# Performance work log

Hardware: AMD Instinct MI355X
Metric: run time of the kernel (lower is better)

Reference implementation:

```python
import jax, jax.numpy as jnp
import numpy as np

J = 8      # number of octaves/scales
Q = 8      # first-order wavelets per octave (Q2 = 1 for second order)
T = 65536  # signal support
EPS = 1e-8
XI_MAX = 0.35  # highest wavelet center frequency (cycles/sample)


def _build_filters(N=T, J_=J, Q_=Q):
    """Morlet-like analytic filterbank defined directly in the Fourier domain."""
    f = np.fft.fftfreq(N)  # normalized freqs in [-0.5, 0.5)
    # first-order: J*Q log-spaced bandpass filters
    xis1 = XI_MAX * 2.0 ** (-np.arange(J_ * Q_) / Q_)
    sig1 = xis1 / Q_
    psi1 = np.exp(-0.5 * ((f[None, :] - xis1[:, None]) / sig1[:, None]) ** 2)
    j1 = np.arange(J_ * Q_) // Q_  # octave index of each first-order filter
    # second-order: one wavelet per octave (Q2=1)
    xis2 = XI_MAX * 2.0 ** (-np.arange(J_).astype(np.float64))
    sig2 = 0.6 * xis2
    psi2 = np.exp(-0.5 * ((f[None, :] - xis2[:, None]) / sig2[:, None]) ** 2)
    # low-pass at scale 2^J
    sig_phi = XI_MAX * 2.0 ** (-J_)
    phi = np.exp(-0.5 * (f / sig_phi) ** 2)
    return (jnp.asarray(psi1, jnp.float32), jnp.asarray(psi2, jnp.float32),
            jnp.asarray(phi, jnp.float32), j1)


def _scatter(x):
    """Order-0/1/2 wavelet scattering: FFT conv -> modulus -> low-pass -> subsample."""
    psi1, psi2, phi, j1 = _build_filters()
    stride = 2 ** J
    xf = jnp.fft.fft(x)  # [B, N] complex64
    lowpass = lambda uf: jnp.real(jnp.fft.ifft(uf * phi))[..., ::stride]
    S0 = lowpass(xf)[:, None, :]                                  # [B, 1, N/2^J]
    U1 = jnp.abs(jnp.fft.ifft(xf[:, None, :] * psi1[None]))      # [B, JQ, N]
    U1f = jnp.fft.fft(U1)
    S1 = lowpass(U1f)                                             # [B, JQ, N/2^J]
    parts = [S0, S1]
    for j2_ in range(J):  # small fixed loop over second-order scales
        sel = j1 < j2_    # static (numpy) frequency-ordering mask
        if not sel.any():
            continue
        U2 = jnp.abs(jnp.fft.ifft(U1f[:, sel] * psi2[j2_]))
        parts.append(lowpass(jnp.fft.fft(U2)))
    return jnp.concatenate(parts, axis=1)  # [B, 289, N/2^J]


def setup_inputs() -> dict:
    key = jax.random.key(0)
    x = jax.random.normal(key, (8, T), dtype=jnp.float32)
    return {"x": x}


def reference(x):
    Sx = _scatter(x)
    # kymatio Scattering1D has no `output_format` attr -> real=Sx, imag=0,
    # then log-magnitude normalization (normalize=True):
    mag = jnp.sqrt(Sx * Sx + EPS)
    real = jnp.log(mag + EPS)
    imag = jnp.zeros_like(real)
    return (real, imag)
```

## Files before the change

kernel.cpp:

```cpp
#include <hip/hip_runtime.h>
#include <hip/hip_fp16.h>
#include <math.h>

#define NN 65536
#define TWO_PI 6.283185307179586f
#define RSTR 264
#define SWZ(m) ((m) ^ (((m) >> 4) & 15))
#define SWZI(m, r) (SWZ(m) ^ ((r) & 12))
#define CTOT 10829824ul

__constant__ int CLO[8]  = {-32768, -15360, -5376, -8192, -8192, -2048, -2048, -2048};
__constant__ int CWW[8]  = {65536, 42240, 16384, 16384, 16384, 4096, 4096, 4096};
__constant__ int CRING[8] = {0, 0, 1, 1, 1, 1, 1, 1};
__constant__ unsigned long COFF[8] = {0ul, 4194304ul, 6897664ul, 7946240ul,
                                      8994816ul, 10043392ul, 10305536ul, 10567680ul};

__device__ __forceinline__ void lds_fence() {
    asm volatile("s_waitcnt lgkmcnt(0)" ::: "memory");
}
__device__ __forceinline__ int rev16(int p) { return ((p & 3) << 2) | (p >> 2); }
__device__ __forceinline__ int rev64(int p) { return ((p & 3) << 4) | (p & 12) | (p >> 4); }

__device__ __forceinline__ int quarter_mask(int klo, int khi)
{
    int qm = 0;
#pragma unroll
    for (int qq = 0; qq < 4; ++qq) {
        int lo_q = 16384 * qq - 255;
        int hi_q = 16384 * qq + 16639;
        bool act;
        if (klo >= 0) act = (hi_q >= klo) && (lo_q <= khi);
        else          act = (lo_q <= khi) || (hi_q >= klo + NN);
        if (act) qm |= (1 << qq);
    }
    return qm;
}

__device__ __forceinline__ void build_tw6(float* twt, int t)
{
    if (t < 16) {
        float s1, c1; __sincosf((TWO_PI / 64.0f) * (float)t, &s1, &c1);
        float c2 = c1 * c1 - s1 * s1, s2 = 2.f * c1 * s1;
        float c3 = c2 * c1 - s2 * s1, s3 = c2 * s1 + s2 * c1;
        float* e = twt + 6 * t;
        e[0] = c1; e[1] = s1; e[2] = c2; e[3] = s2; e[4] = c3; e[5] = s3;
    }
}

template<int SIGN>
__device__ __forceinline__ void fft16(float* xr, float* xi, float* yr, float* yi)
{
    const float S = (SIGN > 0) ? 1.0f : -1.0f;
    const float C8 = 0.92387953251f, S8 = 0.38268343236f, R2 = 0.70710678119f;
#pragma unroll
    for (int n0 = 0; n0 < 4; ++n0) {
        float z0r=xr[n0],    z0i=xi[n0];
        float z1r=xr[n0+4],  z1i=xi[n0+4];
        float z2r=xr[n0+8],  z2i=xi[n0+8];
        float z3r=xr[n0+12], z3i=xi[n0+12];
        float t0r=z0r+z2r, t0i=z0i+z2i;
        float t1r=z0r-z2r, t1i=z0i-z2i;
        float t2r=z1r+z3r, t2i=z1i+z3i;
        float t3r=S*(z1r-z3r), t3i=S*(z1i-z3i);
        xr[n0]=t0r+t2r;      xi[n0]=t0i+t2i;
        xr[n0+4]=t1r-t3i;    xi[n0+4]=t1i+t3r;
        xr[n0+8]=t0r-t2r;    xi[n0+8]=t0i-t2i;
        xr[n0+12]=t1r+t3i;   xi[n0+12]=t1i-t3r;
    }
    {
        const float W1r=C8,  W1i=S*S8;
        const float W2r=R2,  W2i=S*R2;
        const float W3r=S8,  W3i=S*C8;
        const float W6r=-R2, W6i=S*R2;
        const float W9r=-C8, W9i=-S*S8;
#define TWID(idx, wr, wi) { float ar=xr[idx], ai=xi[idx]; xr[idx]=ar*(wr)-ai*(wi); xi[idx]=ar*(wi)+ai*(wr); }
        TWID(5,W1r,W1i)  TWID(9,W2r,W2i)   TWID(13,W3r,W3i)
        TWID(6,W2r,W2i)  { float ar=xr[10], ai=xi[10]; xr[10]=-S*ai; xi[10]=S*ar; } TWID(14,W6r,W6i)
        TWID(7,W3r,W3i)  TWID(11,W6r,W6i)  TWID(15,W9r,W9i)
#undef TWID
    }
#pragma unroll
    for (int p = 0; p < 4; ++p) {
        float z0r=xr[4*p],   z0i=xi[4*p];
        float z1r=xr[4*p+1], z1i=xi[4*p+1];
        float z2r=xr[4*p+2], z2i=xi[4*p+2];
        float z3r=xr[4*p+3], z3i=xi[4*p+3];
        float t0r=z0r+z2r, t0i=z0i+z2i;
        float t1r=z0r-z2r, t1i=z0i-z2i;
        float t2r=z1r+z3r, t2i=z1i+z3i;
        float t3r=S*(z1r-z3r), t3i=S*(z1i-z3i);
        yr[p]=t0r+t2r;     yi[p]=t0i+t2i;
        yr[p+4]=t1r-t3i;   yi[p+4]=t1i+t3r;
        yr[p+8]=t0r-t2r;   yi[p+8]=t0i-t2i;
        yr[p+12]=t1r+t3i;  yi[p+12]=t1i-t3r;
    }
}

template<int SIGN, bool BIGTW, int OUT, bool INREAL, int PADL, int PADR>
__device__ __forceinline__ void fft256_soa(float* rr, float* ri, int u, int n1,
                                           float twrate, float mscale, int cxor, int qmask)
{
    float xr[16], xi[16], yr[16], yi[16];
#pragma unroll
    for (int qq = 0; qq < 4; ++qq) {
        if (qmask & (1 << qq)) {
#pragma unroll
            for (int j = 0; j < 4; ++j) {
                int b = qq * 4 + j;
                int s = SWZ(u + (b << 4)) ^ cxor;
                xr[b] = rr[s];
                xi[b] = INREAL ? 0.f : ri[s];
            }
        } else {
#pragma unroll
            for (int j = 0; j < 4; ++j) { xr[qq * 4 + j] = 0.f; xi[qq * 4 + j] = 0.f; }
        }
    }
    fft16<SIGN>(xr, xi, yr, yi);
    float sa, ca;
    __sincosf((float)SIGN * (TWO_PI / 256.0f) * (float)u, &sa, &ca);
    float twr = 1.f, twi = 0.f;
#pragma unroll
    for (int c = 0; c < 16; ++c) {
        int s = SWZ((c << 4) + u) ^ cxor;
        rr[s] = yr[c] * twr - yi[c] * twi;
        ri[s] = yr[c] * twi + yi[c] * twr;
        float nr = twr * ca - twi * sa; twi = twr * sa + twi * ca; twr = nr;
    }
    lds_fence();
#pragma unroll
    for (int a = 0; a < 16; ++a) {
        int s = SWZ((u << 4) + a) ^ cxor;
        xr[a] = rr[s]; xi[a] = ri[s];
    }
    fft16<SIGN>(xr, xi, yr, yi);
    float tbr = 1.f, tbi = 0.f, str = 1.f, sti = 0.f;
    if (BIGTW) {
        float s0, c0, s1, c1;
        __sincosf((float)SIGN * twrate * (float)(n1 * u), &s0, &c0);
        __sincosf((float)SIGN * twrate * (float)(n1 << 4), &s1, &c1);
        tbr = c0; tbi = s0; str = c1; sti = s1;
    }
#pragma unroll
    for (int d = 0; d < 16; ++d) {
        float vr = yr[d], vi = yi[d];
        if (BIGTW) {
            float pr = vr * tbr - vi * tbi, pi = vr * tbi + vi * tbr;
            vr = pr; vi = pi;
            float nr = tbr * str - tbi * sti; tbi = tbr * sti + tbi * str; tbr = nr;
        }
        int k = u + (d << 4);
        if (OUT == 1) {
            rr[SWZ(k) ^ cxor] = sqrtf(fmaf(vr, vr, vi * vi)) * mscale;
        } else if (OUT == 2) {
            float mag = sqrtf(fmaf(vr, vr, vi * vi)) * mscale;
            ri[PADL + k] = mag;
            if (k >= 256 - PADL) ri[k - (256 - PADL)] = mag;
            if (k < PADR) ri[PADL + 256 + k] = mag;
        } else {
            int s = SWZ(k) ^ cxor;
            rr[s] = vr; ri[s] = vi;
        }
    }
    lds_fence();
}

template<int L, int CLOG, int RST, int SIGN, bool SWZC>
__device__ __forceinline__ void lds_dit(float* re, float* im, const float* twt, int t, int T)
{
    const float S = (float)SIGN;
    const int NC = 1 << CLOG;
    const int nbf = NC * (L >> 2);
    for (int h = 1; h < L; h <<= 2) {
        __syncthreads();
        for (int i = t; i < nbf; i += T) {
            int c = i & (NC - 1);
            int bf = i >> CLOG;
            int j = bf & (h - 1);
            int q0 = ((bf - j) << 2) + j;
            int r0 = q0, r1 = q0 + h, r2 = q0 + 2 * h, r3 = q0 + 3 * h;
            int a0, a1, a2, a3;
            if (SWZC) {
                a0 = r0 * RST + SWZI(c, r0); a1 = r1 * RST + SWZI(c, r1);
                a2 = r2 * RST + SWZI(c, r2); a3 = r3 * RST + SWZI(c, r3);
            } else {
                a0 = r0 * RST + c; a1 = r1 * RST + c; a2 = r2 * RST + c; a3 = r3 * RST + c;
            }
            float x0r = re[a0], x0i = im[a0];
            float x1r = re[a1], x1i = im[a1];
            float x2r = re[a2], x2i = im[a2];
            float x3r = re[a3], x3i = im[a3];
            if (h > 1) {
                const float* e = twt + 6 * (j * (16 / h));
                float cj = e[0], sj = S * e[1];
                float c2 = e[2], s2 = S * e[3];
                float c3 = e[4], s3 = S * e[5];
                float r;
                r = x1r * cj - x1i * sj; x1i = x1r * sj + x1i * cj; x1r = r;
                r = x2r * c2 - x2i * s2; x2i = x2r * s2 + x2i * c2; x2r = r;
                r = x3r * c3 - x3i * s3; x3i = x3r * s3 + x3i * c3; x3r = r;
            }
            float t0r = x0r + x2r, t0i = x0i + x2i;
            float t1r = x0r - x2r, t1i = x0i - x2i;
            float t2r = x1r + x3r, t2i = x1i + x3i;
            float t3r = -S * (x1i - x3i), t3i = S * (x1r - x3r);
            re[a0] = t0r + t2r; im[a0] = t0i + t2i;
            re[a1] = t1r + t3r; im[a1] = t1i + t3i;
            re[a2] = t0r - t2r; im[a2] = t0i - t2i;
            re[a3] = t1r - t3r; im[a3] = t1i - t3i;
        }
    }
    __syncthreads();
}

template<int L, int CLOG, int RST, int SIGN, bool SWZC>
__device__ __forceinline__ void lds_dif(float* re, float* im, const float* twt, int t, int T)
{
    const float S = (float)SIGN;
    const int NC = 1 << CLOG;
    const int nbf = NC * (L >> 2);
    for (int h = L >> 2; h >= 1; h >>= 2) {
        __syncthreads();
        for (int i = t; i < nbf; i += T) {
            int c = i & (NC - 1);
            int bf = i >> CLOG;
            int j = bf & (h - 1);
            int q0 = ((bf - j) << 2) + j;
            int r0 = q0, r1 = q0 + h, r2 = q0 + 2 * h, r3 = q0 + 3 * h;
            int a0, a1, a2, a3;
            if (SWZC) {
                a0 = r0 * RST + SWZI(c, r0); a1 = r1 * RST + SWZI(c, r1);
                a2 = r2 * RST + SWZI(c, r2); a3 = r3 * RST + SWZI(c, r3);
            } else {
                a0 = r0 * RST + c; a1 = r1 * RST + c; a2 = r2 * RST + c; a3 = r3 * RST + c;
            }
            float x0r = re[a0], x0i = im[a0];
            float x1r = re[a1], x1i = im[a1];
            float x2r = re[a2], x2i = im[a2];
            float x3r = re[a3], x3i = im[a3];
            float t0r = x0r + x2r, t0i = x0i + x2i;
            float t1r = x0r - x2r, t1i = x0i - x2i;
            float t2r = x1r + x3r, t2i = x1i + x3i;
            float t3r = -S * (x1i - x3i), t3i = S * (x1r - x3r);
            float y1r = t1r + t3r, y1i = t1i + t3i;
            float y2r = t0r - t2r, y2i = t0i - t2i;
            float y3r = t1r - t3r, y3i = t1i - t3i;
            re[a0] = t0r + t2r; im[a0] = t0i + t2i;
            if (h > 1) {
                const float* e = twt + 6 * (j * (16 / h));
                float cj = e[0], sj = S * e[1];
                float c2 = e[2], s2 = S * e[3];
                float c3 = e[4], s3 = S * e[5];
                re[a1] = y1r * cj - y1i * sj; im[a1] = y1r * sj + y1i * cj;
                re[a2] = y2r * c2 - y2i * s2; im[a2] = y2r * s2 + y2i * c2;
                re[a3] = y3r * c3 - y3i * s3; im[a3] = y3r * s3 + y3i * c3;
            } else {
                re[a1] = y1r; im[a1] = y1i;
                re[a2] = y2r; im[a2] = y2i;
                re[a3] = y3r; im[a3] = y3i;
            }
        }
    }
    __syncthreads();
}

__global__ __launch_bounds__(256)
void xf_stage1(const float* __restrict__ x, float2* __restrict__ D)
{
    __shared__ float sre[16 * RSTR];
    __shared__ float sim[16 * RSTR];
    const int t = threadIdx.x;
    const int r = blockIdx.x >> 4;
    const int n10 = (blockIdx.x & 15) << 4;
#pragma unroll
    for (int it = 0; it < 16; ++it) {
        int flat = it * 256 + t;
        int i = flat & 15, n2 = flat >> 4;
        int n = (n10 + i) + (n2 << 8);
        sre[i * RSTR + SWZI(n2, i)] = x[(size_t)r * NN + n];
        sim[i * RSTR + SWZI(n2, i)] = 0.f;
    }
    __syncthreads();
    const int g = t >> 4, u = t & 15;
    fft256_soa<-1, true, 0, false, 0, 0>(sre + g * RSTR, sim + g * RSTR, u, n10 + g,
                                         TWO_PI / (float)NN, 1.f, g & 12, 15);
    __syncthreads();
#pragma unroll
    for (int it = 0; it < 16; ++it) {
        int flat = it * 256 + t;
        int i = flat & 15, k2 = flat >> 4;
        int s = i * RSTR + SWZI(k2, i);
        D[(size_t)r * NN + (k2 << 8) + (n10 + i)] = make_float2(sre[s], sim[s]);
    }
}

__global__ __launch_bounds__(256)
void xf_stage2(const float2* __restrict__ D, float2* __restrict__ XF)
{
    __shared__ float sre[16 * RSTR];
    __shared__ float sim[16 * RSTR];
    const int t = threadIdx.x;
    const int r = blockIdx.x >> 4;
    const int k20 = (blockIdx.x & 15) << 4;
#pragma unroll
    for (int it = 0; it < 16; ++it) {
        float2 v = D[(size_t)r * NN + ((size_t)(k20 + it) << 8) + t];
        sre[it * RSTR + SWZI(t, it)] = v.x;
        sim[it * RSTR + SWZI(t, it)] = v.y;
    }
    __syncthreads();
    const int g = t >> 4, u = t & 15;
    fft256_soa<-1, false, 0, false, 0, 0>(sre + g * RSTR, sim + g * RSTR, u, 0, 0.f, 1.f, g & 12, 15);
    __syncthreads();
#pragma unroll
    for (int it = 0; it < 16; ++it) {
        int flat = it * 256 + t;
        int fi = flat & 15, k1 = flat >> 4;
        int s = fi * RSTR + SWZI(k1, fi);
        XF[(size_t)r * NN + (size_t)(k20 + fi) + ((size_t)k1 << 8)] = make_float2(sre[s], sim[s]);
    }
}

__global__ __launch_bounds__(256)
void fo_stage1(const float2* __restrict__ XF, __half2* __restrict__ Dh, int qbase)
{
    __shared__ float sre[16 * RSTR];
    __shared__ float sim[16 * RSTR];
    const int t = threadIdx.x;
    const int r = blockIdx.x >> 4;
    const int n10 = (blockIdx.x & 15) << 4;
    const int q = qbase + r;
    const int j1 = q >> 6, ql = q & 63;
    const int srow = ql >> 3, w = ql & 7;
    const int lam = j1 * 8 + w;
    const float xi = 0.35f * exp2f(-(float)lam * 0.125f);
    const float invsig = 8.0f / xi;
    const float kc = xi * (float)NN;
    const float Hh = 5.0f * (xi * 0.125f) * (float)NN;
    const int klo = (int)(kc - Hh), khi = (int)(kc + Hh) + 1;
    const int qm = (khi >= NN) ? 15 : quarter_mask(klo, khi);
#pragma unroll
    for (int it = 0; it < 16; ++it) {
        int i = t & 15, n2 = (it << 4) + (t >> 4);
        if (!(qm & (1 << (it >> 2)))) {
            sre[i * RSTR + SWZI(n2, i)] = 0.f;
            sim[i * RSTR + SWZI(n2, i)] = 0.f;
            continue;
        }
        int n = (n10 + i) + (n2 << 8);
        float nsf = (float)((n < NN / 2) ? n : n - NN);
        float vr = 0.f, vi = 0.f;
        if (fabsf(nsf - kc) <= Hh) {
            float2 v = XF[(size_t)srow * NN + n];
            float a = (nsf * (1.0f / (float)NN) - xi) * invsig;
            float wg = __expf(-0.5f * a * a) * 0.0625f;
            vr = v.x * wg; vi = v.y * wg;
        }
        sre[i * RSTR + SWZI(n2, i)] = vr;
        sim[i * RSTR + SWZI(n2, i)] = vi;
    }
    __syncthreads();
    const int g = t >> 4, u = t & 15;
    fft256_soa<1, true, 0, false, 0, 0>(sre + g * RSTR, sim + g * RSTR, u, n10 + g,
                                        TWO_PI / (float)NN, 1.f, g & 12, qm);
    __syncthreads();
#pragma unroll
    for (int it = 0; it < 16; ++it) {
        int flat = it * 256 + t;
        int i = flat & 15, k2 = flat >> 4;
        int s = i * RSTR + SWZI(k2, i);
        Dh[(size_t)r * NN + (k2 << 8) + (n10 + i)] = __floats2half2_rn(sre[s], sim[s]);
    }
}

__global__ __launch_bounds__(256)
void fo_mid(const __half2* __restrict__ Dh, __half2* __restrict__ D2h)
{
    __shared__ float sre[16 * RSTR];
    __shared__ float sim[16 * RSTR];
    const int t = threadIdx.x;
    const int r = blockIdx.x >> 4;
    const int k20 = (blockIdx.x & 15) << 4;
#pragma unroll
    for (int it = 0; it < 16; ++it) {
        float2 v = __half22float2(Dh[(size_t)r * NN + ((size_t)(k20 + it) << 8) + t]);
        sre[it * RSTR + SWZI(t, it)] = v.x;
        sim[it * RSTR + SWZI(t, it)] = v.y;
    }
    __syncthreads();
    const int g = t >> 4, u = t & 15;
    float* rr = sre + g * RSTR; float* ri = sim + g * RSTR;
    fft256_soa<1, false, 1, false, 0, 0>(rr, ri, u, 0, 0.f, 16.0f / (float)NN, g & 12, 15);
    fft256_soa<-1, true, 0, true, 0, 0>(rr, ri, u, k20 + g, TWO_PI / (float)NN, 1.f, g & 12, 15);
    __syncthreads();
#pragma unroll
    for (int it = 0; it < 16; ++it) {
        int flat = it * 256 + t;
        int i = flat & 15, k2 = flat >> 4;
        int s = i * RSTR + SWZI(k2, i);
        D2h[(size_t)r * NN + (k2 << 8) + (k20 + i)] = __floats2half2_rn(sre[s], sim[s]);
    }
}

__global__ __launch_bounds__(256)
void fo_stage2(const __half2* __restrict__ D2h, __half2* __restrict__ Cw, int qbase)
{
    __shared__ float sre[16 * RSTR];
    __shared__ float sim[16 * RSTR];
    const int t = threadIdx.x;
    const int r = blockIdx.x >> 4;
    const int k20 = (blockIdx.x & 15) << 4;
    const int q = qbase + r;
    const int j1 = q >> 6, ql = q & 63;
#pragma unroll
    for (int it = 0; it < 16; ++it) {
        float2 v = __half22float2(D2h[(size_t)r * NN + ((size_t)(k20 + it) << 8) + t]);
        sre[it * RSTR + SWZI(t, it)] = v.x;
        sim[it * RSTR + SWZI(t, it)] = v.y;
    }
    __syncthreads();
    const int g = t >> 4, u = t & 15;
    fft256_soa<-1, false, 0, false, 0, 0>(sre + g * RSTR, sim + g * RSTR, u, 0, 0.f, 1.f, g & 12, 15);
    __syncthreads();
    const size_t base = COFF[j1] + (size_t)ql * CWW[j1];
    const int lo = CLO[j1], Wd = CWW[j1];
#pragma unroll
    for (int it = 0; it < 16; ++it) {
        int flat = it * 256 + t;
        int fi = flat & 15, k1 = flat >> 4;
        int k = (k20 + fi) + (k1 << 8);
        int ksg = (k < NN / 2) ? k : k - NN;
        int idx = ksg - lo;
        if (idx >= 0 && idx < Wd) {
            int s = fi * RSTR + SWZI(k1, fi);
            Cw[base + idx] = __floats2half2_rn(sre[s], sim[s]);
        }
    }
}

__global__ __launch_bounds__(256)
void sfold_all(const float2* __restrict__ XF, const __half2* __restrict__ Cw,
               float* __restrict__ out)
{
    __shared__ float Gr[256];
    __shared__ float Gi[256];
    const int blk = blockIdx.x;
    const int t = threadIdx.x;
    const float invsigphi = 731.428571f;
    float ar = 0.f, ai = 0.f;
    if (blk < 8) {
#pragma unroll
        for (int qq = -4; qq <= 4; ++qq) {
            int ks = t + (qq << 8);
            int k = ks & (NN - 1);
            float a = ((float)ks * (1.0f / (float)NN)) * invsigphi;
            float wg = __expf(-0.5f * a * a);
            float2 v = XF[(size_t)blk * NN + k];
            ar = fmaf(v.x, wg, ar); ai = fmaf(v.y, wg, ai);
        }
    } else {
        int q = blk - 8;
        int j1 = q >> 6, ql = q & 63;
        size_t base = COFF[j1] + (size_t)ql * CWW[j1];
        int lo = CLO[j1], Wd = CWW[j1], ring = CRING[j1];
#pragma unroll
        for (int qq = -4; qq <= 4; ++qq) {
            int ks = t + (qq << 8);
            float a = ((float)ks * (1.0f / (float)NN)) * invsigphi;
            float wg = __expf(-0.5f * a * a);
            int idx = ring ? ((ks - lo) & (Wd - 1)) : (ks - lo);
            float2 v = __half22float2(Cw[base + idx]);
            ar = fmaf(v.x, wg, ar); ai = fmaf(v.y, wg, ai);
        }
    }
    Gr[t] = ar; Gi[t] = ai;
    __syncthreads();
    float sb, cb;
    __sincosf((TWO_PI / 256.0f) * (float)t, &sb, &cb);
    float wr = 1.f, wi = 0.f, s = 0.f;
    for (int kk = 0; kk < 256; ++kk) {
        s = fmaf(Gr[kk], wr, s);
        s = fmaf(-Gi[kk], wi, s);
        float nr = wr * cb - wi * sb; wi = wr * sb + wi * cb; wr = nr;
    }
    s *= (1.0f / (float)NN);
    float mag = sqrtf(fmaf(s, s, 1e-8f));
    float val = logf(mag + 1e-8f);
    int b, chan;
    if (blk < 8) { b = blk; chan = 0; }
    else { int q = blk - 8; int j1 = q >> 6, ql = q & 63; b = ql >> 3; chan = 1 + j1 * 8 + (ql & 7); }
    out[((size_t)b * 289 + chan) * 256 + t] = val;
}

__device__ __forceinline__ void so_decode_full(int q, int& j1, int& j2, int& rb)
{
    int pp = q >> 6;
    rb = q & 63;
    j2 = (pp == 0) ? 1 : 2;
    j1 = (pp == 0) ? 0 : pp - 1;
}
__device__ __forceinline__ void so_decode_dec16(int q, int& j1, int& j2, int& rb)
{
    int pp = q >> 6;
    rb = q & 63;
    j2 = (pp < 3) ? 3 : 4;
    j1 = (pp < 3) ? pp : pp - 3;
}

__global__ __launch_bounds__(256)
void so_stage1(const __half2* __restrict__ Cw, __half2* __restrict__ Dh, int qbase)
{
    __shared__ float sre[16 * RSTR];
    __shared__ float sim[16 * RSTR];
    const int t = threadIdx.x;
    const int r = blockIdx.x >> 4;
    const int n10 = (blockIdx.x & 15) << 4;
    int j1, j2, rb;
    so_decode_full(qbase + r, j1, j2, rb);
    const float xi2 = 0.35f * exp2f(-(float)j2);
    const float invsig = 1.0f / (0.6f * xi2);
    const float kc = xi2 * (float)NN;
    const float Hh = 5.0f * (0.6f * xi2) * (float)NN;
    const int klo = (int)(kc - Hh), khi = (int)(kc + Hh) + 1;
    const int qm = (klo >= 0 && khi >= NN) ? 15 : quarter_mask(klo, khi);
    const size_t base = COFF[j1] + (size_t)rb * CWW[j1];
    const int lo = CLO[j1], Wd = CWW[j1];
#pragma unroll
    for (int it = 0; it < 16; ++it) {
        int i = t & 15, n2 = (it << 4) + (t >> 4);
        if (!(qm & (1 << (it >> 2)))) {
            sre[i * RSTR + SWZI(n2, i)] = 0.f;
            sim[i * RSTR + SWZI(n2, i)] = 0.f;
            continue;
        }
        int n = (n10 + i) + (n2 << 8);
        int ksg = (n < NN / 2) ? n : n - NN;
        float nsf = (float)ksg;
        float vr = 0.f, vi = 0.f;
        int idx = ksg - lo;
        if (fabsf(nsf - kc) <= Hh && idx >= 0 && idx < Wd) {
            float2 v = __half22float2(Cw[base + idx]);
            float a = (nsf * (1.0f / (float)NN) - xi2) * invsig;
            float wg = __expf(-0.5f * a * a) * (1.0f / 256.0f);
            vr = v.x * wg; vi = v.y * wg;
        }
        sre[i * RSTR + SWZI(n2, i)] = vr;
        sim[i * RSTR + SWZI(n2, i)] = vi;
    }
    __syncthreads();
    const int g = t >> 4, u = t & 15;
    fft256_soa<1, true, 0, false, 0, 0>(sre + g * RSTR, sim + g * RSTR, u, n10 + g,
                                        TWO_PI / (float)NN, 1.f, g & 12, qm);
    __syncthreads();
#pragma unroll
    for (int it = 0; it < 16; ++it) {
        int flat = it * 256 + t;
        int i = flat & 15, k2 = flat >> 4;
        int s = i * RSTR + SWZI(k2, i);
        Dh[(size_t)r * NN + (k2 << 8) + (n10 + i)] = __floats2half2_rn(sre[s], sim[s]);
    }
}

__global__ __launch_bounds__(256)
void so_stage2(const __half2* __restrict__ Dh, float* __restrict__ S2acc, int qbase)
{
    __shared__ float sre[16 * RSTR];
    __shared__ float sim[16 * RSTR];
    __shared__ float wtab[16][8];
    const int t = threadIdx.x;
    const int r = blockIdx.x >> 4;
    const int k20 = (blockIdx.x & 15) << 4;
#pragma unroll
    for (int it = 0; it < 16; ++it) {
        float2 v = __half22float2(Dh[(size_t)r * NN + ((size_t)(k20 + it) << 8) + t]);
        sre[it * RSTR + SWZI(t, it)] = v.x;
        sim[it * RSTR + SWZI(t, it)] = v.y;
    }
    if (t < 128) {
        int fi = t >> 3, dd = (t & 7) - 4;
        int w = k20 + fi + (dd << 8) + 768;
        float val = 0.f;
        if (w >= 0 && w <= 1536) {
            float m = (float)(w - 768);
            val = 0.003426963f * __expf(-3.690276e-5f * m * m);
        }
        wtab[fi][t & 7] = val;
    }
    __syncthreads();
    const int g = t >> 4, u = t & 15;
    fft256_soa<1, false, 2, false, 4, 3>(sre + g * RSTR, sim + g * RSTR, u, 0, 0.f, 1.f, g & 12, 15);
    __syncthreads();
    float acc = 0.f;
#pragma unroll
    for (int fi = 0; fi < 16; ++fi) {
        const float* row = sim + fi * RSTR;
#pragma unroll
        for (int dd = 0; dd < 8; ++dd)
            acc = fmaf(row[t + dd], wtab[fi][dd], acc);
    }
    atomicAdd(&S2acc[(size_t)(qbase + r) * 256 + t], acc * (1.0f / 256.0f));
}

template<int MODE>
__global__ __launch_bounds__(256)
void dec16_s1(const float2* __restrict__ XF, const __half2* __restrict__ Cw,
              __half2* __restrict__ Dh16, int qbase)
{
    __shared__ float sre[64 * 64];
    __shared__ float sim[64 * 64];
    __shared__ float twt[96];
    const int t = threadIdx.x;
    const int r = blockIdx.x >> 2;
    const int c0 = (blockIdx.x & 3) << 6;
    const int q = qbase + r;
    float xi, invsig, kc, Hh; int srow = 0; size_t cbase = 0; int lo = 0, Wd = 0, ring = 0;
    if (MODE == 1) {
        int j1 = 2 + (q >> 6); int ql = q & 63; srow = ql >> 3;
        int lam = j1 * 8 + (ql & 7);
        xi = 0.35f * exp2f(-(float)lam * 0.125f);
        invsig = 8.0f / xi; kc = xi * (float)NN; Hh = 6.10f * (xi * 0.125f) * (float)NN;
    } else {
        int j1, j2, rb;
        so_decode_dec16(q, j1, j2, rb);
        xi = 0.35f * exp2f(-(float)j2);
        invsig = 1.0f / (0.6f * xi); kc = xi * (float)NN;
        Hh = fminf(6.10f * (0.6f * xi) * (float)NN, 7967.0f);
        cbase = COFF[j1] + (size_t)rb * CWW[j1]; lo = CLO[j1]; Wd = CWW[j1]; ring = CRING[j1];
    }
    build_tw6(twt, t);
    const int klo = (int)ceilf(kc - Hh);
#pragma unroll
    for (int it = 0; it < 16; ++it) {
        int flat = it * 256 + t;
        int c = flat & 63, n2 = flat >> 6;
        int kap = (c0 + c) + (n2 << 8);
        int kk = klo + (int)(((unsigned)(kap - klo)) & 16383u);
        float vr = 0.f, vi = 0.f;
        if (fabsf((float)kk - kc) <= Hh) {
            float2 v;
            bool ok = true;
            if (MODE == 1) v = XF[(size_t)srow * NN + (kk & (NN - 1))];
            else {
                int idx;
                if (ring) idx = (kk - lo) & (Wd - 1);
                else { idx = kk - lo; ok = (idx >= 0 && idx < Wd); }
                v = ok ? __half22float2(Cw[cbase + idx]) : make_float2(0.f, 0.f);
            }
            float a = ((float)kk * (1.0f / (float)NN) - xi) * invsig;
            float wg = __expf(-0.5f * a * a) * 0.015625f;
            vr = v.x * wg; vi = v.y * wg;
        }
        int p = rev64(n2);
        sre[(p << 6) + c] = vr;
        sim[(p << 6) + c] = vi;
    }
    lds_dit<64, 6, 64, 1, false>(sre, sim, twt, t, 256);
    {
        const int c = t & 63, r0 = t >> 6;
        float sA, cA, sD, cD;
        __sincosf((TWO_PI / 16384.0f) * (float)(r0 * (c0 + c)), &sA, &cA);
        __sincosf((TWO_PI / 16384.0f) * (float)(4 * (c0 + c)), &sD, &cD);
#pragma unroll
        for (int it = 0; it < 16; ++it) {
            int row = (it << 2) + r0;
            int a = (row << 6) + c;
            float rr = sre[a] * cA - sim[a] * sA;
            sim[a] = sre[a] * sA + sim[a] * cA; sre[a] = rr;
            float nc = cA * cD - sA * sD; sA = cA * sD + sA * cD; cA = nc;
        }
    }
    __syncthreads();
#pragma unroll
    for (int it = 0; it < 16; ++it) {
        int flat = it * 256 + t;
        int c = flat & 63, row = flat >> 6;
        Dh16[(size_t)r * 16384 + (row << 8) + (c0 + c)] =
            __floats2half2_rn(sre[(row << 6) + c], sim[(row << 6) + c]);
    }
}

__global__ __launch_bounds__(256)
void dec16_s2so(const __half2* __restrict__ Dh16, float* __restrict__ S2acc, int qbase)
{
    __shared__ float sre[16 * RSTR];
    __shared__ float sim[16 * RSTR];
    __shared__ float wtab[16][6];
    const int t = threadIdx.x;
    const int r = blockIdx.x >> 2;
    const int k2base = (blockIdx.x & 3) << 4;
#pragma unroll
    for (int it = 0; it < 16; ++it) {
        float2 v = __half22float2(Dh16[(size_t)r * 16384 + ((k2base + it) << 8) + t]);
        sre[it * RSTR + SWZI(t, it)] = v.x;
        sim[it * RSTR + SWZI(t, it)] = v.y;
    }
    if (t < 96) {
        int p = t / 6, dl = t % 6;
        float w = (float)(256 * (dl - 2) - 4 * (k2base + p));
        wtab[p][dl] = 0.003426963f * __expf(-3.690276e-5f * w * w);
    }
    __syncthreads();
    const int g = t >> 4, u = t & 15;
    fft256_soa<1, false, 2, false, 3, 2>(sre + g * RSTR, sim + g * RSTR, u, 0, 0.f,
                                         64.0f / (float)NN, g & 12, 15);
    __syncthreads();
    float acc = 0.f;
#pragma unroll
    for (int p = 0; p < 16; ++p) {
        const float* row = sim + p * RSTR;
#pragma unroll
        for (int dl = 0; dl < 6; ++dl)
            acc = fmaf(row[t + 5 - dl], wtab[p][dl], acc);
    }
    atomicAdd(&S2acc[(size_t)(192 + qbase + r) * 256 + t], acc * 4.0f);
}

__global__ __launch_bounds__(256)
void dec16_s2fo(const __half2* __restrict__ Dh16, __half2* __restrict__ D2h16)
{
    __shared__ float sre[16 * RSTR];
    __shared__ float sim[16 * RSTR];
    const int t = threadIdx.x;
    const int r = blockIdx.x >> 2;
    const int k2base = (blockIdx.x & 3) << 4;
#pragma unroll
    for (int it = 0; it < 16; ++it) {
        float2 v = __half22float2(Dh16[(size_t)r * 16384 + ((k2base + it) << 8) + t]);
        sre[it * RSTR + SWZI(t, it)] = v.x;
        sim[it * RSTR + SWZI(t, it)] = v.y;
    }
    __syncthreads();
    const int g = t >> 4, u = t & 15;
    float* rr = sre + g * RSTR; float* ri = sim + g * RSTR;
    fft256_soa<1, false, 1, false, 0, 0>(rr, ri, u, 0, 0.f, 256.0f / (float)NN, g & 12, 15);
    fft256_soa<-1, true, 0, true, 0, 0>(rr, ri, u, k2base + g, TWO_PI / 16384.0f, 1.f, g & 12, 15);
    __syncthreads();
#pragma unroll
    for (int it = 0; it < 16; ++it) {
        int a = it * RSTR + SWZI(t, it);
        D2h16[(size_t)r * 16384 + ((k2base + it) << 8) + t] = __floats2half2_rn(sre[a], sim[a]);
    }
}

__global__ __launch_bounds__(256)
void dec16_s3fo(const __half2* __restrict__ D2h16, __half2* __restrict__ Cw, int qbase)
{
    __shared__ float sre[64 * 64];
    __shared__ float sim[64 * 64];
    __shared__ float twt[96];
    const int t = threadIdx.x;
    const int r = blockIdx.x >> 2;
    const int c0 = (blockIdx.x & 3) << 6;
    const int q = qbase + r;
    const int j1 = 2 + (q >> 6), ql = q & 63;
    build_tw6(twt, t);
#pragma unroll
    for (int it = 0; it < 16; ++it) {
        int flat = it * 256 + t;
        int c = flat & 63, m2 = flat >> 6;
        float2 v = __half22float2(D2h16[(size_t)r * 16384 + (m2 << 8) + (c0 + c)]);
        sre[(m2 << 6) + c] = v.x;
        sim[(m2 << 6) + c] = v.y;
    }
    lds_dif<64, 6, 64, -1, false>(sre, sim, twt, t, 256);
    const int lo = CLO[j1];
    const size_t rbase = COFF[j1] + (size_t)ql * 16384;
#pragma unroll
    for (int it = 0; it < 16; ++it) {
        int flat = it * 256 + t;
        int c = flat & 63, p = flat >> 6;
        int kap = (c0 + c) + (rev64(p) << 8);
        int ks = (kap < 8192) ? kap : kap - 16384;
        int idx = (ks - lo) & 16383;
        int a = (p << 6) + c;
        Cw[rbase + idx] = __floats2half2_rn(sre[a], sim[a]);
    }
}

__global__ __launch_bounds__(256)
void m4k_fo(const float2* __restrict__ XF, __half2* __restrict__ Cw)
{
    __shared__ float sre[16 * RSTR];
    __shared__ float sim[16 * RSTR];
    __shared__ float twt[96];
    const int t = threadIdx.x;
    const int q = blockIdx.x;
    const int j1 = 5 + (q >> 6), ql = q & 63;
    const int srow = ql >> 3;
    const int lam = j1 * 8 + (ql & 7);
    const float xi = 0.35f * exp2f(-(float)lam * 0.125f);
    const float invsig = 8.0f / xi;
    const float kc = xi * (float)NN;
    const float Hh = 6.10f * (xi * 0.125f) * (float)NN;
    const int klo = (int)ceilf(kc - Hh);
    build_tw6(twt, t);
#pragma unroll
    for (int it = 0; it < 16; ++it) {
        int kap = t + (it << 8);
        int kk = klo + (int)(((unsigned)(kap - klo)) & 4095u);
        float vr = 0.f, vi = 0.f;
        if (fabsf((float)kk - kc) <= Hh) {
            float2 v = XF[(size_t)srow * NN + (kk & (NN - 1))];
            float a = ((float)kk * (1.0f / (float)NN) - xi) * invsig;
            float wg = __expf(-0.5f * a * a);
            vr = v.x * wg; vi = v.y * wg;
        }
        int p = rev16(it);
        sre[p * RSTR + SWZI(t, p)] = vr;
        sim[p * RSTR + SWZI(t, p)] = vi;
    }
    lds_dit<16, 8, RSTR, 1, true>(sre, sim, twt, t, 256);
    {
        float sD, cD; __sincosf((TWO_PI / 4096.0f) * (float)t, &sD, &cD);
        float cA = 1.f, sA = 0.f;
#pragma unroll
        for (int it = 0; it < 16; ++it) {
            int a = it * RSTR + SWZI(t, it);
            float rr = sre[a] * cA - sim[a] * sA;
            sim[a] = sre[a] * sA + sim[a] * cA; sre[a] = rr;
            float nc = cA * cD - sA * sD; sA = cA * sD + sA * cD; cA = nc;
        }
    }
    __syncthreads();
    const int g = t >> 4, u = t & 15;
    float* rr = sre + g * RSTR; float* ri = sim + g * RSTR;
    fft256_soa<1, false, 1, false, 0, 0>(rr, ri, u, 0, 0.f, 16.0f / (float)NN, g & 12, 15);
    fft256_soa<-1, true, 0, true, 0, 0>(rr, ri, u, g, TWO_PI / 4096.0f, 1.f, g & 12, 15);
    lds_dif<16, 8, RSTR, -1, true>(sre, sim, twt, t, 256);
    const int lo = CLO[j1];
    const size_t rbase = COFF[j1] + (size_t)ql * 4096;
#pragma unroll
    for (int it = 0; it < 16; ++it) {
        int kap = t + (rev16(it) << 8);
        int ks = (kap < 2048) ? kap : kap - 4096;
        int idx = (ks - lo) & 4095;
        int a = it * RSTR + SWZI(t, it);
        Cw[rbase + idx] = __floats2half2_rn(sre[a], sim[a]);
    }
}

__global__ __launch_bounds__(256)
void m4k_so(const __half2* __restrict__ Cw, float* __restrict__ out)
{
    __shared__ float sre[16 * RSTR];
    __shared__ float sim[16 * RSTR];
    __shared__ float wtab[16][6];
    __shared__ float twt[96];
    const int t = threadIdx.x;
    const int q = blockIdx.x;
    const int pp = q >> 6, rb = q & 63;
    int j1, j2;
    if (pp < 5)       { j2 = 5; j1 = pp; }
    else if (pp < 11) { j2 = 6; j1 = pp - 5; }
    else              { j2 = 7; j1 = pp - 11; }
    const float xi2 = 0.35f * exp2f(-(float)j2);
    const float invsig = 1.0f / (0.6f * xi2);
    const float kc = xi2 * (float)NN;
    const float Hh = fminf(6.10f * (0.6f * xi2) * (float)NN, 1823.0f);
    const int klo = (int)ceilf(kc - Hh);
    const size_t cbase = COFF[j1] + (size_t)rb * CWW[j1];
    const int lo = CLO[j1], Wd = CWW[j1], ring = CRING[j1];
    build_tw6(twt, t);
#pragma unroll
    for (int it = 0; it < 16; ++it) {
        int kap = t + (it << 8);
        int kk = klo + (int)(((unsigned)(kap - klo)) & 4095u);
        float vr = 0.f, vi = 0.f;
        if (fabsf((float)kk - kc) <= Hh) {
            int idx; bool ok = true;
            if (ring) idx = (kk - lo) & (Wd - 1);
            else { idx = kk - lo; ok = (idx >= 0 && idx < Wd); }
            if (ok) {
                float2 v = __half22float2(Cw[cbase + idx]);
                float a = ((float)kk * (1.0f / (float)NN) - xi2) * invsig;
                float wg = __expf(-0.5f * a * a);
                vr = v.x * wg; vi = v.y * wg;
            }
        }
        int p = rev16(it);
        sre[p * RSTR + SWZI(t, p)] = vr;
        sim[p * RSTR + SWZI(t, p)] = vi;
    }
    if (t < 96) {
        int p = t / 6, dl = t % 6;
        float w = (float)(256 * (dl - 2) - 16 * p);
        wtab[p][dl] = 0.003426963f * __expf(-3.690276e-5f * w * w);
    }
    lds_dit<16, 8, RSTR, 1, true>(sre, sim, twt, t, 256);
    {
        float sD, cD; __sincosf((TWO_PI / 4096.0f) * (float)t, &sD, &cD);
        float cA = 1.f, sA = 0.f;
#pragma unroll
        for (int it = 0; it < 16; ++it) {
            int a = it * RSTR + SWZI(t, it);
            float rr = sre[a] * cA - sim[a] * sA;
            sim[a] = sre[a] * sA + sim[a] * cA; sre[a] = rr;
            float nc = cA * cD - sA * sD; sA = cA * sD + sA * cD; cA = nc;
        }
    }
    __syncthreads();
    const int g = t >> 4, u = t & 15;
    fft256_soa<1, false, 2, false, 3, 2>(sre + g * RSTR, sim + g * RSTR, u, 0, 0.f,
                                         1.0f / (float)NN, g & 12, 15);
    __syncthreads();
    float acc = 0.f;
#pragma unroll
    for (int p = 0; p < 16; ++p) {
        const float* row = sim + p * RSTR;
#pragma unroll
        for (int dl = 0; dl < 6; ++dl)
            acc = fmaf(row[t + 5 - dl], wtab[p][dl], acc);
    }
    acc *= 16.0f;
    const int b = rb >> 3;
    const int chan = 65 + 4 * j2 * (j2 - 1) + j1 * 8 + (rb & 7);
    float mag = sqrtf(fmaf(acc, acc, 1e-8f));
    out[((size_t)b * 289 + chan) * 256 + t] = logf(mag + 1e-8f);
}

__global__ __launch_bounds__(256)
void s2final(const float* __restrict__ S2acc, float* __restrict__ out)
{
    const int q = blockIdx.x, n = threadIdx.x;
    int j1, j2, rb;
    if (q < 192) so_decode_full(q, j1, j2, rb);
    else         so_decode_dec16(q - 192, j1, j2, rb);
    const int b = rb >> 3;
    const int chan = 65 + 4 * j2 * (j2 - 1) + j1 * 8 + (rb & 7);
    float s = S2acc[(size_t)q * 256 + n];
    float mag = sqrtf(fmaf(s, s, 1e-8f));
    out[((size_t)b * 289 + chan) * 256 + n] = logf(mag + 1e-8f);
}

__global__ void zero2_kernel(float* a, int na, float* b, int nb)
{
    int i = blockIdx.x * 256 + threadIdx.x;
    if (i < na) a[i] = 0.f;
    else if (i < na + nb) b[i - na] = 0.f;
}

extern "C" void kernel_launch(void* const* d_in, const int* in_sizes, int n_in,
                              void* d_out, int out_size, void* d_ws, size_t ws_size,
                              hipStream_t stream)
{
    const float* x = (const float*)d_in[0];
    float* out = (float*)d_out;
    char* ws = (char*)d_ws;

    size_t off = 0;
    float2*  XF    = (float2*)ws;                 off += 8ul * NN * 8;
    __half2* Cw    = (__half2*)(ws + off);        off += CTOT * 4ul;
    float*   S2acc = (float*)(ws + off);          off += 640ul * 256 * 4;
    off = (off + 255) & ~255ul;
    char* reg0 = ws + off;
    size_t avail = (ws_size > off) ? (ws_size - off) : 0;

    int CHB = (int)(avail / (512ul * 1024));  if (CHB > 128) CHB = 128;  if (CHB < 1) CHB = 1;
    int CHD = (int)(avail / (256ul * 1024));  if (CHD > 192) CHD = 192;  if (CHD < 1) CHD = 1;
    int CHE = (int)(avail / (128ul * 1024));  if (CHE > 192) CHE = 192;  if (CHE < 1) CHE = 1;
    int CHF = (int)(avail / (64ul * 1024));   if (CHF > 448) CHF = 448;  if (CHF < 1) CHF = 1;

    {
        int nz = 8 * 289 * 256;
        int na = 640 * 256;
        zero2_kernel<<<(nz + na + 255) / 256, 256, 0, stream>>>(out + nz, nz, S2acc, na);
    }

    {
        float2* Df = (float2*)reg0;
        xf_stage1<<<8 * 16, 256, 0, stream>>>(x, Df);
        xf_stage2<<<8 * 16, 256, 0, stream>>>(Df, XF);
    }

    for (int cs = 0; cs < 128; cs += CHB) {
        int m = (128 - cs < CHB) ? (128 - cs) : CHB;
        __half2* DhB = (__half2*)reg0;
        __half2* D2h = DhB + (size_t)CHB * NN;
        fo_stage1<<<m * 16, 256, 0, stream>>>(XF, DhB, cs);
        fo_mid<<<m * 16, 256, 0, stream>>>(DhB, D2h);
        fo_stage2<<<m * 16, 256, 0, stream>>>(D2h, Cw, cs);
    }
    for (int cs = 0; cs < 192; cs += CHE) {
        int m = (192 - cs < CHE) ? (192 - cs) : CHE;
        __half2* Dh16  = (__half2*)reg0;
        __half2* D2h16 = Dh16 + (size_t)CHE * 16384;
        dec16_s1<1><<<m * 4, 256, 0, stream>>>(XF, Cw, Dh16, cs);
        dec16_s2fo<<<m * 4, 256, 0, stream>>>(Dh16, D2h16);
        dec16_s3fo<<<m * 4, 256, 0, stream>>>(D2h16, Cw, cs);
    }
    m4k_fo<<<192, 256, 0, stream>>>(XF, Cw);

    sfold_all<<<8 + 512, 256, 0, stream>>>(XF, Cw, out);

    for (int qs = 0; qs < 192; qs += CHD) {
        int m = (192 - qs < CHD) ? (192 - qs) : CHD;
        __half2* DhS = (__half2*)reg0;
        so_stage1<<<m * 16, 256, 0, stream>>>(Cw, DhS, qs);
        so_stage2<<<m * 16, 256, 0, stream>>>(DhS, S2acc, qs);
    }
    for (int qs = 0; qs < 448; qs += CHF) {
        int m = (448 - qs < CHF) ? (448 - qs) : CHF;
        __half2* Dh16 = (__half2*)reg0;
        dec16_s1<2><<<m * 4, 256, 0, stream>>>(XF, Cw, Dh16, qs);
        dec16_s2so<<<m * 4, 256, 0, stream>>>(Dh16, S2acc, qs);
    }
    m4k_so<<<1152, 256, 0, stream>>>(Cw, out);

    s2final<<<640, 256, 0, stream>>>(S2acc, out);
}
```

Before: 308.1 us.

## Merge independent stage kernels into horizontally fused launches with fixed scratch layout

Converts each stage kernel into a device function and dispatches them from a few combined kernels by block-index range, so independent first- and second-order pipelines (m4k, dec16, full-resolution paths, sfold) run in the same launch. It also drops the workspace-dependent chunking loops and uses fixed scratch offsets. The aim is fewer launches and less tail idling, with better GPU fill from running independent work together. In exchange every branch gets the largest shared-memory allocation, which can lower occupancy, and the code assumes the workspace is large enough for the full intermediates.

```diff
diff --git a/kernel.cpp b/kernel.cpp
--- a/kernel.cpp
+++ b/kernel.cpp
@@ -321,15 +321,13 @@
     }
 }
 
-__global__ __launch_bounds__(256)
-void fo_stage1(const float2* __restrict__ XF, __half2* __restrict__ Dh, int qbase)
-{
-    __shared__ float sre[16 * RSTR];
-    __shared__ float sim[16 * RSTR];
-    const int t = threadIdx.x;
-    const int r = blockIdx.x >> 4;
-    const int n10 = (blockIdx.x & 15) << 4;
-    const int q = qbase + r;
+__device__ void d_fo_stage1(float* sm, int t, int blk, const float2* __restrict__ XF,
+                            __half2* __restrict__ Dh)
+{
+    float* sre = sm; float* sim = sm + 4224;
+    const int r = blk >> 4;
+    const int n10 = (blk & 15) << 4;
+    const int q = r;
     const int j1 = q >> 6, ql = q & 63;
     const int srow = ql >> 3, w = ql & 7;
     const int lam = j1 * 8 + w;
@@ -373,14 +371,12 @@
     }
 }
 
-__global__ __launch_bounds__(256)
-void fo_mid(const __half2* __restrict__ Dh, __half2* __restrict__ D2h)
-{
-    __shared__ float sre[16 * RSTR];
-    __shared__ float sim[16 * RSTR];
-    const int t = threadIdx.x;
-    const int r = blockIdx.x >> 4;
-    const int k20 = (blockIdx.x & 15) << 4;
+__device__ void d_fo_mid(float* sm, int t, int blk, const __half2* __restrict__ Dh,
+                         __half2* __restrict__ D2h)
+{
+    float* sre = sm; float* sim = sm + 4224;
+    const int r = blk >> 4;
+    const int k20 = (blk & 15) << 4;
 #pragma unroll
     for (int it = 0; it < 16; ++it) {
         float2 v = __half22float2(Dh[(size_t)r * NN + ((size_t)(k20 + it) << 8) + t]);
@@ -402,16 +398,13 @@
     }
 }
 
-__global__ __launch_bounds__(256)
-void fo_stage2(const __half2* __restrict__ D2h, __half2* __restrict__ Cw, int qbase)
-{
-    __shared__ float sre[16 * RSTR];
-    __shared__ float sim[16 * RSTR];
-    const int t = threadIdx.x;
-    const int r = blockIdx.x >> 4;
-    const int k20 = (blockIdx.x & 15) << 4;
-    const int q = qbase + r;
-    const int j1 = q >> 6, ql = q & 63;
+__device__ void d_fo_stage2(float* sm, int t, int blk, const __half2* __restrict__ D2h,
+                            __half2* __restrict__ Cw)
+{
+    float* sre = sm; float* sim = sm + 4224;
+    const int r = blk >> 4;
+    const int k20 = (blk & 15) << 4;
+    const int j1 = r >> 6, ql = r & 63;
 #pragma unroll
     for (int it = 0; it < 16; ++it) {
         float2 v = __half22float2(D2h[(size_t)r * NN + ((size_t)(k20 + it) << 8) + t]);
@@ -438,14 +431,10 @@
     }
 }
 
-__global__ __launch_bounds__(256)
-void sfold_all(const float2* __restrict__ XF, const __half2* __restrict__ Cw,
-               float* __restrict__ out)
-{
-    __shared__ float Gr[256];
-    __shared__ float Gi[256];
-    const int blk = blockIdx.x;
-    const int t = threadIdx.x;
+__device__ void d_sfold(float* sm, int t, int blk, const float2* __restrict__ XF,
+                        const __half2* __restrict__ Cw, float* __restrict__ out)
+{
+    float* Gr = sm; float* Gi = sm + 256;
     const float invsigphi = 731.428571f;
     float ar = 0.f, ai = 0.f;
     if (blk < 8) {
@@ -507,16 +496,14 @@
     j1 = (pp < 3) ? pp : pp - 3;
 }
 
-__global__ __launch_bounds__(256)
-void so_stage1(const __half2* __restrict__ Cw, __half2* __restrict__ Dh, int qbase)
-{
-    __shared__ float sre[16 * RSTR];
-    __shared__ float sim[16 * RSTR];
-    const int t = threadIdx.x;
-    const int r = blockIdx.x >> 4;
-    const int n10 = (blockIdx.x & 15) << 4;
+__device__ void d_so_stage1(float* sm, int t, int blk, const __half2* __restrict__ Cw,
+                            __half2* __restrict__ Dh)
+{
+    float* sre = sm; float* sim = sm + 4224;
+    const int r = blk >> 4;
+    const int n10 = (blk & 15) << 4;
     int j1, j2, rb;
-    so_decode_full(qbase + r, j1, j2, rb);
+    so_decode_full(r, j1, j2, rb);
     const float xi2 = 0.35f * exp2f(-(float)j2);
     const float invsig = 1.0f / (0.6f * xi2);
     const float kc = xi2 * (float)NN;
@@ -561,15 +548,13 @@
     }
 }
 
-__global__ __launch_bounds__(256)
-void so_stage2(const __half2* __restrict__ Dh, float* __restrict__ S2acc, int qbase)
-{
-    __shared__ float sre[16 * RSTR];
-    __shared__ float sim[16 * RSTR];
-    __shared__ float wtab[16][8];
-    const int t = threadIdx.x;
-    const int r = blockIdx.x >> 4;
-    const int k20 = (blockIdx.x & 15) << 4;
+__device__ void d_so_stage2(float* sm, int t, int blk, const __half2* __restrict__ Dh,
+                            float* __restrict__ S2acc)
+{
+    float* sre = sm; float* sim = sm + 4224;
+    float* wtab = sm + 8448;
+    const int r = blk >> 4;
+    const int k20 = (blk & 15) << 4;
 #pragma unroll
     for (int it = 0; it < 16; ++it) {
         float2 v = __half22float2(Dh[(size_t)r * NN + ((size_t)(k20 + it) << 8) + t]);
@@ -584,7 +569,7 @@
             float m = (float)(w - 768);
             val = 0.003426963f * __expf(-3.690276e-5f * m * m);
         }
-        wtab[fi][t & 7] = val;
+        wtab[fi * 8 + (t & 7)] = val;
     }
     __syncthreads();
     const int g = t >> 4, u = t & 15;
@@ -596,23 +581,19 @@
         const float* row = sim + fi * RSTR;
 #pragma unroll
         for (int dd = 0; dd < 8; ++dd)
-            acc = fmaf(row[t + dd], wtab[fi][dd], acc);
-    }
-    atomicAdd(&S2acc[(size_t)(qbase + r) * 256 + t], acc * (1.0f / 256.0f));
+            acc = fmaf(row[t + dd], wtab[fi * 8 + dd], acc);
+    }
+    atomicAdd(&S2acc[(size_t)r * 256 + t], acc * (1.0f / 256.0f));
 }
 
 template<int MODE>
-__global__ __launch_bounds__(256)
-void dec16_s1(const float2* __restrict__ XF, const __half2* __restrict__ Cw,
-              __half2* __restrict__ Dh16, int qbase)
-{
-    __shared__ float sre[64 * 64];
-    __shared__ float sim[64 * 64];
-    __shared__ float twt[96];
-    const int t = threadIdx.x;
-    const int r = blockIdx.x >> 2;
-    const int c0 = (blockIdx.x & 3) << 6;
-    const int q = qbase + r;
+__device__ void d_dec16_s1(float* sm, int t, int blk, const float2* __restrict__ XF,
+                           const __half2* __restrict__ Cw, __half2* __restrict__ Dh16)
+{
+    float* sre = sm; float* sim = sm + 4096; float* twt = sm + 8192;
+    const int r = blk >> 2;
+    const int c0 = (blk & 3) << 6;
+    const int q = r;
     float xi, invsig, kc, Hh; int srow = 0; size_t cbase = 0; int lo = 0, Wd = 0, ring = 0;
     if (MODE == 1) {
         int j1 = 2 + (q >> 6); int ql = q & 63; srow = ql >> 3;
@@ -679,15 +660,13 @@
     }
 }
 
-__global__ __launch_bounds__(256)
-void dec16_s2so(const __half2* __restrict__ Dh16, float* __restrict__ S2acc, int qbase)
-{
-    __shared__ float sre[16 * RSTR];
-    __shared__ float sim[16 * RSTR];
-    __shared__ float wtab[16][6];
-    const int t = threadIdx.x;
-    const int r = blockIdx.x >> 2;
-    const int k2base = (blockIdx.x & 3) << 4;
+__device__ void d_dec16_s2so(float* sm, int t, int blk, const __half2* __restrict__ Dh16,
+                             float* __restrict__ S2acc)
+{
+    float* sre = sm; float* sim = sm + 4224;
+    float* wtab = sm + 8448;
+    const int r = blk >> 2;
+    const int k2base = (blk & 3) << 4;
 #pragma unroll
     for (int it = 0; it < 16; ++it) {
         float2 v = __half22float2(Dh16[(size_t)r * 16384 + ((k2base + it) << 8) + t]);
@@ -697,7 +676,7 @@
     if (t < 96) {
         int p = t / 6, dl = t % 6;
         float w = (float)(256 * (dl - 2) - 4 * (k2base + p));
-        wtab[p][dl] = 0.003426963f * __expf(-3.690276e-5f * w * w);
+        wtab[p * 6 + dl] = 0.003426963f * __expf(-3.690276e-5f * w * w);
     }
     __syncthreads();
     const int g = t >> 4, u = t & 15;
@@ -710,19 +689,17 @@
         const float* row = sim + p * RSTR;
 #pragma unroll
         for (int dl = 0; dl < 6; ++dl)
-            acc = fmaf(row[t + 5 - dl], wtab[p][dl], acc);
-    }
-    atomicAdd(&S2acc[(size_t)(192 + qbase + r) * 256 + t], acc * 4.0f);
-}
-
-__global__ __launch_bounds__(256)
-void dec16_s2fo(const __half2* __restrict__ Dh16, __half2* __restrict__ D2h16)
-{
-    __shared__ float sre[16 * RSTR];
-    __shared__ float sim[16 * RSTR];
-    const int t = threadIdx.x;
-    const int r = blockIdx.x >> 2;
-    const int k2base = (blockIdx.x & 3) << 4;
+            acc = fmaf(row[t + 5 - dl], wtab[p * 6 + dl], acc);
+    }
+    atomicAdd(&S2acc[(size_t)(192 + r) * 256 + t], acc * 4.0f);
+}
+
+__device__ void d_dec16_s2fo(float* sm, int t, int blk, const __half2* __restrict__ Dh16,
+                             __half2* __restrict__ D2h16)
+{
+    float* sre = sm; float* sim = sm + 4224;
+    const int r = blk >> 2;
+    const int k2base = (blk & 3) << 4;
 #pragma unroll
     for (int it = 0; it < 16; ++it) {
         float2 v = __half22float2(Dh16[(size_t)r * 16384 + ((k2base + it) << 8) + t]);
@@ -742,17 +719,13 @@
     }
 }
 
-__global__ __launch_bounds__(256)
-void dec16_s3fo(const __half2* __restrict__ D2h16, __half2* __restrict__ Cw, int qbase)
-{
-    __shared__ float sre[64 * 64];
-    __shared__ float sim[64 * 64];
-    __shared__ float twt[96];
-    const int t = threadIdx.x;
-    const int r = blockIdx.x >> 2;
-    const int c0 = (blockIdx.x & 3) << 6;
-    const int q = qbase + r;
-    const int j1 = 2 + (q >> 6), ql = q & 63;
+__device__ void d_dec16_s3fo(float* sm, int t, int blk, const __half2* __restrict__ D2h16,
+                             __half2* __restrict__ Cw)
+{
+    float* sre = sm; float* sim = sm + 4096; float* twt = sm + 8192;
+    const int r = blk >> 2;
+    const int c0 = (blk & 3) << 6;
+    const int j1 = 2 + (r >> 6), ql = r & 63;
     build_tw6(twt, t);
 #pragma unroll
     for (int it = 0; it < 16; ++it) {
@@ -777,14 +750,11 @@
     }
 }
 
-__global__ __launch_bounds__(256)
-void m4k_fo(const float2* __restrict__ XF, __half2* __restrict__ Cw)
-{
-    __shared__ float sre[16 * RSTR];
-    __shared__ float sim[16 * RSTR];
-    __shared__ float twt[96];
-    const int t = threadIdx.x;
-    const int q = blockIdx.x;
+__device__ void d_m4k_fo(float* sm, int t, int blk, const float2* __restrict__ XF,
+                         __half2* __restrict__ Cw)
+{
+    float* sre = sm; float* sim = sm + 4224; float* twt = sm + 8448;
+    const int q = blk;
     const int j1 = 5 + (q >> 6), ql = q & 63;
     const int srow = ql >> 3;
     const int lam = j1 * 8 + (ql & 7);
@@ -839,15 +809,12 @@
     }
 }
 
-__global__ __launch_bounds__(256)
-void m4k_so(const __half2* __restrict__ Cw, float* __restrict__ out)
-{
-    __shared__ float sre[16 * RSTR];
-    __shared__ float sim[16 * RSTR];
-    __shared__ float wtab[16][6];
-    __shared__ float twt[96];
-    const int t = threadIdx.x;
-    const int q = blockIdx.x;
+__device__ void d_m4k_so(float* sm, int t, int blk, const __half2* __restrict__ Cw,
+                         float* __restrict__ out)
+{
+    float* sre = sm; float* sim = sm + 4224;
+    float* twt = sm + 8448; float* wtab = sm + 8544;
+    const int q = blk;
     const int pp = q >> 6, rb = q & 63;
     int j1, j2;
     if (pp < 5)       { j2 = 5; j1 = pp; }
@@ -884,7 +851,7 @@
     if (t < 96) {
         int p = t / 6, dl = t % 6;
         float w = (float)(256 * (dl - 2) - 16 * p);
-        wtab[p][dl] = 0.003426963f * __expf(-3.690276e-5f * w * w);
+        wtab[p * 6 + dl] = 0.003426963f * __expf(-3.690276e-5f * w * w);
     }
     lds_dit<16, 8, RSTR, 1, true>(sre, sim, twt, t, 256);
     {
@@ -909,13 +876,72 @@
         const float* row = sim + p * RSTR;
 #pragma unroll
         for (int dl = 0; dl < 6; ++dl)
-            acc = fmaf(row[t + 5 - dl], wtab[p][dl], acc);
+            acc = fmaf(row[t + 5 - dl], wtab[p * 6 + dl], acc);
     }
     acc *= 16.0f;
     const int b = rb >> 3;
     const int chan = 65 + 4 * j2 * (j2 - 1) + j1 * 8 + (rb & 7);
     float mag = sqrtf(fmaf(acc, acc, 1e-8f));
     out[((size_t)b * 289 + chan) * 256 + t] = logf(mag + 1e-8f);
+}
+
+__global__ __launch_bounds__(256)
+void fo_s1_kernel(const float2* __restrict__ XF, __half2* __restrict__ Cw,
+                  __half2* __restrict__ DhB, __half2* __restrict__ Dh16)
+{
+    __shared__ float sm[8704];
+    const int t = threadIdx.x;
+    const int b = blockIdx.x;
+    if (b < 192) d_m4k_fo(sm, t, b, XF, Cw);
+    else if (b < 960) d_dec16_s1<1>(sm, t, b - 192, XF, nullptr, Dh16);
+    else d_fo_stage1(sm, t, b - 960, XF, DhB);
+}
+
+__global__ __launch_bounds__(256)
+void fo_s2_kernel(const __half2* __restrict__ DhB, const __half2* __restrict__ Dh16,
+                  __half2* __restrict__ D2h, __half2* __restrict__ D2h16)
+{
+    __shared__ float sm[8704];
+    const int t = threadIdx.x;
+    const int b = blockIdx.x;
+    if (b < 768) d_dec16_s2fo(sm, t, b, Dh16, D2h16);
+    else d_fo_mid(sm, t, b - 768, DhB, D2h);
+}
+
+__global__ __launch_bounds__(256)
+void fo_s3_kernel(const __half2* __restrict__ D2h, const __half2* __restrict__ D2h16,
+                  __half2* __restrict__ Cw)
+{
+    __shared__ float sm[8704];
+    const int t = threadIdx.x;
+    const int b = blockIdx.x;
+    if (b < 768) d_dec16_s3fo(sm, t, b, D2h16, Cw);
+    else d_fo_stage2(sm, t, b - 768, D2h, Cw);
+}
+
+__global__ __launch_bounds__(256)
+void so_1_kernel(const float2* __restrict__ XF, const __half2* __restrict__ Cw,
+                 __half2* __restrict__ DhS, __half2* __restrict__ Dh16so,
+                 float* __restrict__ out)
+{
+    __shared__ float sm[8704];
+    const int t = threadIdx.x;
+    const int b = blockIdx.x;
+    if (b < 1152) d_m4k_so(sm, t, b, Cw, out);
+    else if (b < 2944) d_dec16_s1<2>(sm, t, b - 1152, nullptr, Cw, Dh16so);
+    else if (b < 6016) d_so_stage1(sm, t, b - 2944, Cw, DhS);
+    else d_sfold(sm, t, b - 6016, XF, Cw, out);
+}
+
+__global__ __launch_bounds__(256)
+void so_2_kernel(const __half2* __restrict__ DhS, const __half2* __restrict__ Dh16so,
+                 float* __restrict__ S2acc)
+{
+    __shared__ float sm[8704];
+    const int t = threadIdx.x;
+    const int b = blockIdx.x;
+    if (b < 1792) d_dec16_s2so(sm, t, b, Dh16so, S2acc);
+    else d_so_stage2(sm, t, b - 1792, DhS, S2acc);
 }
 
 __global__ __launch_bounds__(256)
@@ -952,13 +978,15 @@
     __half2* Cw    = (__half2*)(ws + off);        off += CTOT * 4ul;
     float*   S2acc = (float*)(ws + off);          off += 640ul * 256 * 4;
     off = (off + 255) & ~255ul;
-    char* reg0 = ws + off;
-    size_t avail = (ws_size > off) ? (ws_size - off) : 0;
-
-    int CHB = (int)(avail / (512ul * 1024));  if (CHB > 128) CHB = 128;  if (CHB < 1) CHB = 1;
-    int CHD = (int)(avail / (256ul * 1024));  if (CHD > 192) CHD = 192;  if (CHD < 1) CHD = 1;
-    int CHE = (int)(avail / (128ul * 1024));  if (CHE > 192) CHE = 192;  if (CHE < 1) CHE = 1;
-    int CHF = (int)(avail / (64ul * 1024));   if (CHF > 448) CHF = 448;  if (CHF < 1) CHF = 1;
+    char* sc = ws + off;
+
+    __half2* DhB   = (__half2*)sc;
+    __half2* D2h   = (__half2*)(sc + 33554432ul);
+    __half2* Dh16  = (__half2*)(sc + 67108864ul);
+    __half2* D2h16 = (__half2*)(sc + 79691776ul);
+    __half2* DhS    = (__half2*)sc;
+    __half2* Dh16so = (__half2*)(sc + 50331648ul);
+    float2*  Df     = (float2*)sc;
 
     {
         int nz = 8 * 289 * 256;
@@ -966,45 +994,14 @@
         zero2_kernel<<<(nz + na + 255) / 256, 256, 0, stream>>>(out + nz, nz, S2acc, na);
     }
 
-    {
-        float2* Df = (float2*)reg0;
-        xf_stage1<<<8 * 16, 256, 0, stream>>>(x, Df);
-        xf_stage2<<<8 * 16, 256, 0, stream>>>(Df, XF);
-    }
-
-    for (int cs = 0; cs < 128; cs += CHB) {
-        int m = (128 - cs < CHB) ? (128 - cs) : CHB;
-        __half2* DhB = (__half2*)reg0;
-        __half2* D2h = DhB + (size_t)CHB * NN;
-        fo_stage1<<<m * 16, 256, 0, stream>>>(XF, DhB, cs);
-        fo_mid<<<m * 16, 256, 0, stream>>>(DhB, D2h);
-        fo_stage2<<<m * 16, 256, 0, stream>>>(D2h, Cw, cs);
-    }
-    for (int cs = 0; cs < 192; cs += CHE) {
-        int m = (192 - cs < CHE) ? (192 - cs) : CHE;
-        __half2* Dh16  = (__half2*)reg0;
-        __half2* D2h16 = Dh16 + (size_t)CHE * 16384;
-        dec16_s1<1><<<m * 4, 256, 0, stream>>>(XF, Cw, Dh16, cs);
-        dec16_s2fo<<<m * 4, 256, 0, stream>>>(Dh16, D2h16);
-        dec16_s3fo<<<m * 4, 256, 0, stream>>>(D2h16, Cw, cs);
-    }
-    m4k_fo<<<192, 256, 0, stream>>>(XF, Cw);
-
-    sfold_all<<<8 + 512, 256, 0, stream>>>(XF, Cw, out);
-
-    for (int qs = 0; qs < 192; qs += CHD) {
-        int m = (192 - qs < CHD) ? (192 - qs) : CHD;
-        __half2* DhS = (__half2*)reg0;
-        so_stage1<<<m * 16, 256, 0, stream>>>(Cw, DhS, qs);
-        so_stage2<<<m * 16, 256, 0, stream>>>(DhS, S2acc, qs);
-    }
-    for (int qs = 0; qs < 448; qs += CHF) {
-        int m = (448 - qs < CHF) ? (448 - qs) : CHF;
-        __half2* Dh16 = (__half2*)reg0;
-        dec16_s1<2><<<m * 4, 256, 0, stream>>>(XF, Cw, Dh16, qs);
-        dec16_s2so<<<m * 4, 256, 0, stream>>>(Dh16, S2acc, qs);
-    }
-    m4k_so<<<1152, 256, 0, stream>>>(Cw, out);
-
+    xf_stage1<<<8 * 16, 256, 0, stream>>>(x, Df);
+    xf_stage2<<<8 * 16, 256, 0, stream>>>(Df, XF);
+
+    fo_s1_kernel<<<3008, 256, 0, stream>>>(XF, Cw, DhB, Dh16);
+    fo_s2_kernel<<<2816, 256, 0, stream>>>(DhB, Dh16, D2h, D2h16);
+    fo_s3_kernel<<<2816, 256, 0, stream>>>(D2h, D2h16, Cw);
+
+    so_1_kernel<<<6536, 256, 0, stream>>>(XF, Cw, DhS, Dh16so, out);
+    so_2_kernel<<<4864, 256, 0, stream>>>(DhS, Dh16so, S2acc);
     s2final<<<640, 256, 0, stream>>>(S2acc, out);
 }
```

Result: faster. 257.6 us (median of 2 runs) (-16.4%).
